# Kernel tuning notes

Measured on AMD Instinct MI355X. Metric: run time of the kernel, lower is better.

The kernel has to match this reference:

```python
import jax, jax.numpy as jnp
import numpy as np

B, S, SE, D, V, L, H = 32, 256, 1024, 512, 8000, 4, 8
EPS = 1e-3   # keras BatchNormalization default epsilon
NEG = -1e9


def _heads(x, W, b):
    Bx, Sx, Dx = x.shape
    return (jnp.einsum('bsd,de->bse', x, W) + b).reshape(Bx, Sx, H, Dx // H).transpose(0, 2, 1, 3)


def mha(q_in, kv_in, Wq, bq, Wk, bk, Wv, bv, Wo, bo, causal):
    dk = q_in.shape[-1] // H
    q = _heads(q_in, Wq, bq)   # [B,H,Sq,dk]
    k = _heads(kv_in, Wk, bk)  # [B,H,Sk,dk]
    v = _heads(kv_in, Wv, bv)
    scores = jnp.einsum('bhqd,bhkd->bhqk', q, k) / jnp.sqrt(jnp.asarray(dk, q.dtype))
    if causal:
        # original loop uses values = x[:, :j, :] -> token j attends to STRICTLY previous tokens;
        # token 0 has zero keys, so its attention output is exactly zero (before Wo bias).
        Sq, Sk = scores.shape[-2], scores.shape[-1]
        mask = jnp.arange(Sk)[None, :] < jnp.arange(Sq)[:, None]
        attn = jax.nn.softmax(jnp.where(mask, scores, NEG), axis=-1)
        attn = jnp.where(mask, attn, 0.0)
    else:
        attn = jax.nn.softmax(scores, axis=-1)
    out = jnp.einsum('bhqk,bhkd->bhqd', attn, v)
    out = out.transpose(0, 2, 1, 3).reshape(q_in.shape[0], q_in.shape[1], -1)
    return out @ Wo + bo


def bn(x, gamma, beta, mean, var):
    # keras BatchNorm, inference mode, axis=-1
    return gamma * (x - mean) * jax.lax.rsqrt(var + EPS) + beta


def setup_inputs():
    key = jax.random.key(0)
    ks = iter(jax.random.split(key, 80))

    def rn(*shape):
        return jax.random.normal(next(ks), shape, jnp.float32) * 0.02

    inp = {
        'sequence': jax.random.randint(next(ks), (B, S), 0, V, jnp.int32),
        'encoder_output': jax.random.normal(next(ks), (B, SE, D), jnp.float32),
        'pos_encodings': jax.random.normal(next(ks), (S, D), jnp.float32),
        'emb': rn(V, D),
        'Wout': rn(D, V), 'bout': jnp.zeros((V,), jnp.float32),
        'W1': rn(L, D, 512), 'b1': jnp.zeros((L, 512), jnp.float32),
        'W2': rn(L, 512, D), 'b2': jnp.zeros((L, D), jnp.float32),
    }
    for p in ('bot', 'mid'):
        for nm in ('Wq', 'Wk', 'Wv', 'Wo'):
            inp[f'{nm}_{p}'] = rn(L, D, D)
        for nm in ('bq', 'bk', 'bv', 'bo'):
            inp[f'{nm}_{p}'] = jnp.zeros((L, D), jnp.float32)
    for p in ('bot', 'mid', 'ffn'):
        inp[f'gamma_{p}'] = jnp.ones((L, D), jnp.float32)
        inp[f'beta_{p}'] = jnp.zeros((L, D), jnp.float32)
        inp[f'mean_{p}'] = jnp.zeros((L, D), jnp.float32)
        inp[f'var_{p}'] = jnp.ones((L, D), jnp.float32)
    return inp


def reference(sequence, encoder_output, pos_encodings, emb, Wout, bout, W1, b1, W2, b2,
              Wq_bot, Wk_bot, Wv_bot, Wo_bot, bq_bot, bk_bot, bv_bot, bo_bot,
              Wq_mid, Wk_mid, Wv_mid, Wo_mid, bq_mid, bk_mid, bv_mid, bo_mid,
              gamma_bot, beta_bot, mean_bot, var_bot,
              gamma_mid, beta_mid, mean_mid, var_mid,
              gamma_ffn, beta_ffn, mean_ffn, var_ffn):
    x = emb[sequence] + pos_encodings[None, :, :]  # [B,S,D]
    for i in range(L):
        a = mha(x, x, Wq_bot[i], bq_bot[i], Wk_bot[i], bk_bot[i], Wv_bot[i], bv_bot[i], Wo_bot[i], bo_bot[i], True)
        x = bn(x + a, gamma_bot[i], beta_bot[i], mean_bot[i], var_bot[i])
        a = mha(x, encoder_output, Wq_mid[i], bq_mid[i], Wk_mid[i], bk_mid[i], Wv_mid[i], bv_mid[i], Wo_mid[i], bo_mid[i], False)
        x = bn(x + a, gamma_mid[i], beta_mid[i], mean_mid[i], var_mid[i])
        f = jax.nn.relu(x @ W1[i] + b1[i]) @ W2[i] + b2[i]
        x = bn(x + f, gamma_ffn[i], beta_ffn[i], mean_ffn[i], var_ffn[i])
    return x @ Wout + bout  # logits [B,S,V]
```

## Files before the change

### kernel.cpp

```cpp
#include <hip/hip_runtime.h>
#include <hip/hip_fp16.h>

typedef _Float16 half8 __attribute__((ext_vector_type(8)));
typedef _Float16 half4 __attribute__((ext_vector_type(4)));
typedef float floatx4 __attribute__((ext_vector_type(4)));

#define NB 32
#define NS 256
#define NSE 1024
#define ND 512
#define NV 8000
#define NVP 8064
#define NL 4
#define NH 8
#define NDK 64
#define BN_EPS 1e-3f

typedef const __attribute__((address_space(1))) void* gas_ptr;
typedef __attribute__((address_space(3))) void* las_ptr;
__device__ __forceinline__ void gload16(const void* g, void* l) {
    __builtin_amdgcn_global_load_lds((gas_ptr)g, (las_ptr)l, 16, 0, 0);
}

__global__ __launch_bounds__(256) void k_cast(const float* __restrict__ in, _Float16* __restrict__ out) {
    size_t i = ((size_t)blockIdx.x * 256 + threadIdx.x) * 8;
    float4 a = *(const float4*)(in + i);
    float4 b = *(const float4*)(in + i + 4);
    half8 o;
    o[0] = (_Float16)a.x; o[1] = (_Float16)a.y; o[2] = (_Float16)a.z; o[3] = (_Float16)a.w;
    o[4] = (_Float16)b.x; o[5] = (_Float16)b.y; o[6] = (_Float16)b.z; o[7] = (_Float16)b.w;
    *(half8*)(out + i) = o;
}

__global__ __launch_bounds__(256) void k_embed(const int* __restrict__ seq,
                                               const float* __restrict__ emb,
                                               const float* __restrict__ pos,
                                               _Float16* __restrict__ x) {
    size_t i = ((size_t)blockIdx.x * 256 + threadIdx.x) * 8;
    int tok = (int)(i / ND);
    int d = (int)(i % ND);
    int s = tok % NS;
    int t = seq[tok];
    const float* ep = emb + (size_t)t * ND + d;
    const float* pp = pos + (size_t)s * ND + d;
    half8 o;
    for (int j = 0; j < 8; j++) o[j] = (_Float16)(ep[j] + pp[j]);
    *(half8*)(x + i) = o;
}

__global__ void k_transpose_w(const float* __restrict__ in, _Float16* __restrict__ out, int R, int C,
                              long long ostride) {
    __shared__ float tile[32][33];
    int b = blockIdx.z;
    int c0 = blockIdx.x * 32, r0 = blockIdx.y * 32;
    const float* pin = in + (size_t)b * R * C;
    _Float16* pout = out + (size_t)b * ostride;
    int tx = threadIdx.x, ty = threadIdx.y;
    for (int j = 0; j < 32; j += 8)
        tile[ty + j][tx] = pin[(size_t)(r0 + ty + j) * C + c0 + tx];
    __syncthreads();
    for (int j = 0; j < 32; j += 8)
        pout[(size_t)(c0 + ty + j) * R + r0 + tx] = (_Float16)tile[tx][ty + j];
}

template<int BM>
__global__ __launch_bounds__(256) void k_gemm(
    const _Float16* __restrict__ A, const _Float16* __restrict__ Bt,
    const float* __restrict__ bias0, const float* __restrict__ bias1, const float* __restrict__ bias2,
    void* __restrict__ C0, void* __restrict__ C1, void* __restrict__ C2,
    int M, int N, int K, int relu, int mode, int Sb,
    const _Float16* __restrict__ xres,
    const float* __restrict__ bng, const float* __restrict__ bnb,
    const float* __restrict__ bnm, const float* __restrict__ bnv) {
    constexpr int BN = 128;
    constexpr int BK = 64;
    constexpr int MI = BM / 32;
    constexpr int BUFH = (BM + BN) * BK;
    constexpr int LA = (BM + BN) / 32;
    __shared__ __align__(16) _Float16 smem[2 * BUFH];

    int tid = threadIdx.x;
    int wid = tid >> 6, lane = tid & 63, quad = lane >> 4, r = lane & 15;

    int nwg = gridDim.x * gridDim.y;
    int orig = blockIdx.y * gridDim.x + blockIdx.x;
    int q8 = nwg >> 3, r8 = nwg & 7;
    int xcd = orig & 7, loc = orig >> 3;
    int swz = (xcd < r8 ? xcd * (q8 + 1) : r8 * (q8 + 1) + (xcd - r8) * q8) + loc;
    int m0 = (swz / gridDim.x) * BM;
    int n0 = (swz % gridDim.x) * BN;

    int wm = (wid >> 1) * (BM / 2);
    int wn = (wid & 1) * 64;

    floatx4 zf = {0.f, 0.f, 0.f, 0.f};
    floatx4 acc[MI][4];
    for (int i = 0; i < MI; i++) for (int j = 0; j < 4; j++) acc[i][j] = zf;

    int srow = wid * 8 + (lane >> 3);
    int scol = (((lane & 7) ^ ((lane >> 3) & 7)) << 3);

    auto stage = [&](int k0, int buf) {
        _Float16* As = smem + buf * BUFH;
        _Float16* Bs = As + BM * BK;
        const _Float16* abase = A + (size_t)(m0 + srow) * K + k0 + scol;
        _Float16* asl = As + (wid * 8) * BK;
#pragma unroll
        for (int i = 0; i < BM / 32; i++)
            gload16(abase + (size_t)(i * 32) * K, asl + (i * 32) * BK);
        const _Float16* bbase = Bt + (size_t)(n0 + srow) * K + k0 + scol;
        _Float16* bsl = Bs + (wid * 8) * BK;
#pragma unroll
        for (int i = 0; i < 4; i++)
            gload16(bbase + (size_t)(i * 32) * K, bsl + (i * 32) * BK);
    };

    int NT = K / BK;
    int cur = 0;
    stage(0, 0);
    for (int t = 0; t < NT; t++) {
        if (t + 1 < NT) {
            stage((t + 1) * BK, cur ^ 1);
            asm volatile("s_waitcnt vmcnt(%0)" :: "n"(LA) : "memory");
        } else {
            asm volatile("s_waitcnt vmcnt(0)" ::: "memory");
        }
        __builtin_amdgcn_s_barrier();
        const _Float16* As = smem + cur * BUFH;
        const _Float16* Bs = As + BM * BK;
#pragma unroll
        for (int ks = 0; ks < BK; ks += 32) {
            half8 af[MI], bg[4];
#pragma unroll
            for (int i = 0; i < MI; i++)
                af[i] = *(const half8*)&As[(wm + i * 16 + r) * BK + ((((ks >> 3) + quad) ^ (r & 7)) << 3)];
#pragma unroll
            for (int j = 0; j < 4; j++)
                bg[j] = *(const half8*)&Bs[(wn + j * 16 + r) * BK + ((((ks >> 3) + quad) ^ (r & 7)) << 3)];
#pragma unroll
            for (int i = 0; i < MI; i++)
#pragma unroll
                for (int j = 0; j < 4; j++)
                    acc[i][j] = __builtin_amdgcn_mfma_f32_16x16x32_f16(af[i], bg[j], acc[i][j], 0, 0, 0);
        }
        if (t + 1 < NT) {
            __builtin_amdgcn_s_barrier();
            cur ^= 1;
        }
    }

    int seg = 0, nloc = n0, om = mode;
    const float* bias = bias0;
    char* C = (char*)C0;
    if (mode == 4) {
        seg = n0 >> 9; nloc = n0 & 511;
        om = (seg == 2) ? 1 : 0;
        C = (char*)(seg == 0 ? C0 : (seg == 1 ? C1 : C2));
        bias = (seg == 0) ? bias0 : ((seg == 1) ? bias1 : bias2);
    } else if (mode == 5) {
        seg = n0 >> 9; nloc = n0 & 511;
        om = seg ? 1 : 0;
        C = (char*)(seg ? C1 : C0);
        bias = seg ? bias1 : bias0;
    }

    if (om == 1) {
        for (int i = 0; i < MI; i++) {
            int grow = m0 + wm + i * 16 + quad * 4;
            int b = grow / Sb, s = grow - b * Sb;
            _Float16* outp = (_Float16*)C + (size_t)b * 512 * Sb + s;
#pragma unroll
            for (int j = 0; j < 4; j++) {
                int cb = nloc + wn + j * 16 + r;
                float bv = bias[cb];
                half4 h;
#pragma unroll
                for (int g = 0; g < 4; g++) h[g] = (_Float16)(acc[i][j][g] + bv);
                *(half4*)(outp + (size_t)cb * Sb) = h;
            }
        }
    } else {
        float* Ep = (float*)(void*)(smem + (cur ^ 1) * BUFH) + wid * (16 * 68);
        int rr = lane >> 4;
        int c = (lane & 15) * 4;
        for (int i = 0; i < MI; i++) {
#pragma unroll
            for (int j = 0; j < 4; j++) {
                int cb = nloc + wn + j * 16 + r;
                float bv = (om == 2) ? (cb < N ? bias[cb] : 0.0f) : bias[cb];
#pragma unroll
                for (int g = 0; g < 4; g++) {
                    float v = acc[i][j][g] + bv;
                    if (relu) v = fmaxf(v, 0.0f);
                    Ep[(quad * 4 + g) * 68 + j * 16 + r] = v;
                }
            }
            int grow0 = m0 + wm + i * 16;
            int cb = nloc + wn + c;
            if (om == 0) {
#pragma unroll
                for (int p = 0; p < 4; p++) {
                    float4 v = *(float4*)&Ep[(p * 4 + rr) * 68 + c];
                    half4 h;
                    h[0] = (_Float16)v.x; h[1] = (_Float16)v.y; h[2] = (_Float16)v.z; h[3] = (_Float16)v.w;
                    *(half4*)&((_Float16*)C)[(size_t)(grow0 + p * 4 + rr) * 512 + cb] = h;
                }
            } else if (om == 3) {
                float4 g4 = *(const float4*)(bng + cb);
                float4 b4 = *(const float4*)(bnb + cb);
                float4 m4 = *(const float4*)(bnm + cb);
                float4 v4 = *(const float4*)(bnv + cb);
                float s0 = g4.x * rsqrtf(v4.x + BN_EPS);
                float s1 = g4.y * rsqrtf(v4.y + BN_EPS);
                float s2 = g4.z * rsqrtf(v4.z + BN_EPS);
                float s3 = g4.w * rsqrtf(v4.w + BN_EPS);
#pragma unroll
                for (int p = 0; p < 4; p++) {
                    int grow = grow0 + p * 4 + rr;
                    float4 v = *(float4*)&Ep[(p * 4 + rr) * 68 + c];
                    half4 xv = *(const half4*)(xres + (size_t)grow * 512 + cb);
                    half4 h;
                    h[0] = (_Float16)((v.x + (float)xv[0] - m4.x) * s0 + b4.x);
                    h[1] = (_Float16)((v.y + (float)xv[1] - m4.y) * s1 + b4.y);
                    h[2] = (_Float16)((v.z + (float)xv[2] - m4.z) * s2 + b4.z);
                    h[3] = (_Float16)((v.w + (float)xv[3] - m4.w) * s3 + b4.w);
                    *(half4*)&((_Float16*)C)[(size_t)grow * 512 + cb] = h;
                }
            } else {
                if (cb < N) {
#pragma unroll
                    for (int p = 0; p < 4; p++) {
                        float4 v = *(float4*)&Ep[(p * 4 + rr) * 68 + c];
                        *(float4*)&((float*)C)[(size_t)(grow0 + p * 4 + rr) * N + cb] = v;
                    }
                }
            }
        }
    }
}

__global__ __launch_bounds__(256) void k_attn(const _Float16* __restrict__ Q, const _Float16* __restrict__ Kb,
                                              const _Float16* __restrict__ Vt, _Float16* __restrict__ O,
                                              int Sk, int causal) {
    __shared__ _Float16 Plds[4][16][72];
    int qt = blockIdx.x, h = blockIdx.y, b = blockIdx.z;
    int tid = threadIdx.x;
    int w = tid >> 6, lane = tid & 63, quad = lane >> 4, r = lane & 15;
    int qbase = qt * 64 + w * 16;

    floatx4 zf = {0.f, 0.f, 0.f, 0.f};
    half8 aq[2];
    const _Float16* qptr = Q + (size_t)(b * NS + qbase + r) * ND + h * NDK;
    aq[0] = *(const half8*)(qptr + quad * 8);
    aq[1] = *(const half8*)(qptr + 32 + quad * 8);

    floatx4 Of[4];
    for (int j = 0; j < 4; j++) Of[j] = zf;
    float mrow[4], lrow[4];
    for (int g = 0; g < 4; g++) { mrow[g] = -1e30f; lrow[g] = 0.0f; }

    int ntiles = causal ? (qt + 1) : (Sk >> 6);

    for (int kt = 0; kt < ntiles; kt++) {
        floatx4 sc[4];
        for (int j = 0; j < 4; j++) sc[j] = zf;
        for (int t = 0; t < 2; t++) {
            for (int j = 0; j < 4; j++) {
                const _Float16* kptr = Kb + (size_t)(b * Sk + kt * 64 + j * 16 + r) * ND + h * NDK + t * 32 + quad * 8;
                half8 bk = *(const half8*)kptr;
                sc[j] = __builtin_amdgcn_mfma_f32_16x16x32_f16(aq[t], bk, sc[j], 0, 0, 0);
            }
        }
        float s[4][4], tmax[4];
        for (int g = 0; g < 4; g++) tmax[g] = -1e30f;
        for (int j = 0; j < 4; j++) {
            int key = kt * 64 + j * 16 + r;
            for (int g = 0; g < 4; g++) {
                float v = sc[j][g] * 0.125f;
                int qi = qbase + quad * 4 + g;
                if (causal && key >= qi) v = -1e30f;
                s[j][g] = v;
                tmax[g] = fmaxf(tmax[g], v);
            }
        }
        for (int off = 1; off < 16; off <<= 1)
            for (int g = 0; g < 4; g++)
                tmax[g] = fmaxf(tmax[g], __shfl_xor(tmax[g], off, 64));
        float alpha[4], psum[4];
        for (int g = 0; g < 4; g++) {
            float mnew = fmaxf(mrow[g], tmax[g]);
            alpha[g] = (mnew <= -1e29f) ? 1.0f : __expf(mrow[g] - mnew);
            mrow[g] = mnew;
            psum[g] = 0.0f;
        }
        for (int j = 0; j < 4; j++) {
            for (int g = 0; g < 4; g++) {
                float p = (s[j][g] <= -1e29f) ? 0.0f : __expf(s[j][g] - mrow[g]);
                psum[g] += p;
                Plds[w][quad * 4 + g][j * 16 + r] = (_Float16)p;
            }
        }
        for (int off = 1; off < 16; off <<= 1)
            for (int g = 0; g < 4; g++)
                psum[g] += __shfl_xor(psum[g], off, 64);
        for (int g = 0; g < 4; g++) lrow[g] = lrow[g] * alpha[g] + psum[g];
        for (int j = 0; j < 4; j++)
            for (int g = 0; g < 4; g++)
                Of[j][g] *= alpha[g];
        __syncthreads();
        for (int t = 0; t < 2; t++) {
            half8 ap = *(const half8*)&Plds[w][r][t * 32 + quad * 8];
            for (int j = 0; j < 4; j++) {
                const _Float16* vptr = Vt + (size_t)((b * NH + h) * NDK + j * 16 + r) * Sk + kt * 64 + t * 32 + quad * 8;
                half8 bv = *(const half8*)vptr;
                Of[j] = __builtin_amdgcn_mfma_f32_16x16x32_f16(ap, bv, Of[j], 0, 0, 0);
            }
        }
        __syncthreads();
    }
    for (int j = 0; j < 4; j++) {
        for (int g = 0; g < 4; g++) {
            int row = qbase + quad * 4 + g;
            float inv = (lrow[g] > 0.f) ? 1.0f / lrow[g] : 0.0f;
            O[(size_t)(b * NS + row) * ND + h * NDK + j * 16 + r] = (_Float16)(Of[j][g] * inv);
        }
    }
}

extern "C" void kernel_launch(void* const* d_in, const int* in_sizes, int n_in,
                              void* d_out, int out_size, void* d_ws, size_t ws_size,
                              hipStream_t stream) {
    const int*   seq  = (const int*)d_in[0];
    const float* enc  = (const float*)d_in[1];
    const float* pos  = (const float*)d_in[2];
    const float* emb  = (const float*)d_in[3];
    const float* Wout = (const float*)d_in[4];
    const float* bout = (const float*)d_in[5];
    const float* W1   = (const float*)d_in[6];
    const float* b1   = (const float*)d_in[7];
    const float* W2   = (const float*)d_in[8];
    const float* b2   = (const float*)d_in[9];
    const float* Wq_bot = (const float*)d_in[10];
    const float* Wk_bot = (const float*)d_in[11];
    const float* Wv_bot = (const float*)d_in[12];
    const float* Wo_bot = (const float*)d_in[13];
    const float* bq_bot = (const float*)d_in[14];
    const float* bk_bot = (const float*)d_in[15];
    const float* bv_bot = (const float*)d_in[16];
    const float* bo_bot = (const float*)d_in[17];
    const float* Wq_mid = (const float*)d_in[18];
    const float* Wk_mid = (const float*)d_in[19];
    const float* Wv_mid = (const float*)d_in[20];
    const float* Wo_mid = (const float*)d_in[21];
    const float* bq_mid = (const float*)d_in[22];
    const float* bk_mid = (const float*)d_in[23];
    const float* bv_mid = (const float*)d_in[24];
    const float* bo_mid = (const float*)d_in[25];
    const float* gam[3] = {(const float*)d_in[26], (const float*)d_in[30], (const float*)d_in[34]};
    const float* bet[3] = {(const float*)d_in[27], (const float*)d_in[31], (const float*)d_in[35]};
    const float* mea[3] = {(const float*)d_in[28], (const float*)d_in[32], (const float*)d_in[36]};
    const float* vr [3] = {(const float*)d_in[29], (const float*)d_in[33], (const float*)d_in[37]};

    char* wp = (char*)d_ws;
    auto alloc = [&](size_t elems) -> _Float16* {
        _Float16* p = (_Float16*)wp;
        wp += ((elems * 2 + 255) / 256) * 256;
        return p;
    };
    const size_t DD = (size_t)ND * ND;
    _Float16* WqkvTb = alloc(NL * 3 * DD);
    _Float16* WoTb   = alloc(NL * DD);
    _Float16* WqTm   = alloc(NL * DD);
    _Float16* WkvTm  = alloc(NL * 2 * DD);
    _Float16* WoTm   = alloc(NL * DD);
    _Float16* W1T    = alloc(NL * DD);
    _Float16* W2T    = alloc(NL * DD);
    _Float16* WoutT  = alloc((size_t)NVP * ND);
    const size_t XSZ = (size_t)NB * NS * ND;
    _Float16* x   = alloc(XSZ);
    _Float16* qb  = alloc(XSZ);
    _Float16* kb  = alloc(XSZ);
    _Float16* vts = alloc(XSZ);
    _Float16* ao  = alloc(XSZ);
    const size_t ESZ = (size_t)NB * NSE * ND;
    _Float16* ench  = alloc(ESZ);
    _Float16* kenc  = alloc(ESZ);
    _Float16* vtenc = alloc(ESZ);

    hipMemsetAsync(WoutT + (size_t)NV * ND, 0, (size_t)(NVP - NV) * ND * sizeof(_Float16), stream);

    dim3 tb(32, 8);
    const long long S1 = (long long)DD, S2 = (long long)(2 * DD), S3 = (long long)(3 * DD);
    k_transpose_w<<<dim3(16, 16, NL), tb, 0, stream>>>(Wq_bot, WqkvTb,          ND, ND, S3);
    k_transpose_w<<<dim3(16, 16, NL), tb, 0, stream>>>(Wk_bot, WqkvTb + DD,     ND, ND, S3);
    k_transpose_w<<<dim3(16, 16, NL), tb, 0, stream>>>(Wv_bot, WqkvTb + 2 * DD, ND, ND, S3);
    k_transpose_w<<<dim3(16, 16, NL), tb, 0, stream>>>(Wo_bot, WoTb,            ND, ND, S1);
    k_transpose_w<<<dim3(16, 16, NL), tb, 0, stream>>>(Wq_mid, WqTm,            ND, ND, S1);
    k_transpose_w<<<dim3(16, 16, NL), tb, 0, stream>>>(Wk_mid, WkvTm,           ND, ND, S2);
    k_transpose_w<<<dim3(16, 16, NL), tb, 0, stream>>>(Wv_mid, WkvTm + DD,      ND, ND, S2);
    k_transpose_w<<<dim3(16, 16, NL), tb, 0, stream>>>(Wo_mid, WoTm,            ND, ND, S1);
    k_transpose_w<<<dim3(16, 16, NL), tb, 0, stream>>>(W1,     W1T,             ND, ND, S1);
    k_transpose_w<<<dim3(16, 16, NL), tb, 0, stream>>>(W2,     W2T,             ND, ND, S1);
    k_transpose_w<<<dim3(NV / 32, 16, 1), tb, 0, stream>>>(Wout, WoutT, ND, NV, S1);
    k_cast<<<dim3((int)(ESZ / 8 / 256)), 256, 0, stream>>>(enc, ench);
    k_embed<<<dim3((int)(XSZ / 8 / 256)), 256, 0, stream>>>(seq, emb, pos, x);

    auto gemm64 = [&](const _Float16* A, const _Float16* Bt, const float* b0, void* Cp,
                      int relu, int mode, const _Float16* xr, const float* g, const float* be,
                      const float* me, const float* ve) {
        k_gemm<64><<<dim3(4, 128), 256, 0, stream>>>(A, Bt, b0, nullptr, nullptr,
            Cp, nullptr, nullptr, 8192, 512, 512, relu, mode, 0, xr, g, be, me, ve);
    };

    for (int l = 0; l < NL; l++) {
        size_t wofs = (size_t)l * DD;
        size_t bofs = (size_t)l * ND;
        k_gemm<128><<<dim3(12, 64), 256, 0, stream>>>(x, WqkvTb + (size_t)l * 3 * DD,
            bq_bot + bofs, bk_bot + bofs, bv_bot + bofs, qb, kb, vts,
            8192, 1536, 512, 0, 4, NS, nullptr, nullptr, nullptr, nullptr, nullptr);
        k_attn<<<dim3(NS / 64, NH, NB), 256, 0, stream>>>(qb, kb, vts, ao, NS, 1);
        gemm64(ao, WoTb + wofs, bo_bot + bofs, x, 0, 3, x,
               gam[0] + bofs, bet[0] + bofs, mea[0] + bofs, vr[0] + bofs);
        gemm64(x, WqTm + wofs, bq_mid + bofs, qb, 0, 0, nullptr, nullptr, nullptr, nullptr, nullptr);
        k_gemm<128><<<dim3(8, 256), 256, 0, stream>>>(ench, WkvTm + (size_t)l * 2 * DD,
            bk_mid + bofs, bv_mid + bofs, nullptr, kenc, vtenc, nullptr,
            32768, 1024, 512, 0, 5, NSE, nullptr, nullptr, nullptr, nullptr, nullptr);
        k_attn<<<dim3(NS / 64, NH, NB), 256, 0, stream>>>(qb, kenc, vtenc, ao, NSE, 0);
        gemm64(ao, WoTm + wofs, bo_mid + bofs, x, 0, 3, x,
               gam[1] + bofs, bet[1] + bofs, mea[1] + bofs, vr[1] + bofs);
        gemm64(x, W1T + wofs, b1 + bofs, qb, 1, 0, nullptr, nullptr, nullptr, nullptr, nullptr);
        gemm64(qb, W2T + wofs, b2 + bofs, x, 0, 3, x,
               gam[2] + bofs, bet[2] + bofs, mea[2] + bofs, vr[2] + bofs);
    }
    k_gemm<128><<<dim3(63, 64), 256, 0, stream>>>(x, WoutT, bout, nullptr, nullptr,
        d_out, nullptr, nullptr, 8192, NV, 512, 0, 2, 0, nullptr, nullptr, nullptr, nullptr, nullptr);
}
```

Measured before the change: 1.765 ms.

## Widen attention KV tiles, stage transposed GEMM stores via LDS, batch weight transposes

Attention now processes 128 keys per tile instead of 64, which halves the number of softmax rescale and barrier iterations. It also fully unrolls the inner loops and raises wave priority around the MFMA sections. The BM=128 GEMM path that writes head-transposed outputs now stages results in swizzled LDS, so each global store becomes a coalesced 16-byte write instead of a strided 8-byte one. The ten per-weight transpose launches are merged into one kernel launch. Costs are higher register pressure from 8 score accumulators and extra causal work on partially masked 128-wide tiles.

```diff
diff --git a/kernel.cpp b/kernel.cpp
--- a/kernel.cpp
+++ b/kernel.cpp
@@ -14,6 +14,7 @@
 #define NL 4
 #define NH 8
 #define NDK 64
+#define KVB 128
 #define BN_EPS 1e-3f
 
 typedef const __attribute__((address_space(1))) void* gas_ptr;
@@ -61,6 +62,26 @@
     __syncthreads();
     for (int j = 0; j < 32; j += 8)
         pout[(size_t)(c0 + ty + j) * R + r0 + tx] = (_Float16)tile[tx][ty + j];
+}
+
+struct TWArgs {
+    const float* src[10];
+    _Float16* dst[10];
+    long long ostride[10];
+};
+__global__ void k_transpose_all(TWArgs a) {
+    __shared__ float tile[32][33];
+    int z = blockIdx.z;
+    int g = z >> 2, l = z & 3;
+    const float* pin = a.src[g] + (size_t)l * ND * ND;
+    _Float16* pout = a.dst[g] + (size_t)l * a.ostride[g];
+    int c0 = blockIdx.x * 32, r0 = blockIdx.y * 32;
+    int tx = threadIdx.x, ty = threadIdx.y;
+    for (int j = 0; j < 32; j += 8)
+        tile[ty + j][tx] = pin[(size_t)(r0 + ty + j) * ND + c0 + tx];
+    __syncthreads();
+    for (int j = 0; j < 32; j += 8)
+        pout[(size_t)(c0 + ty + j) * ND + r0 + tx] = (_Float16)tile[tx][ty + j];
 }
 
 template<int BM>
@@ -165,18 +186,51 @@
     }
 
     if (om == 1) {
-        for (int i = 0; i < MI; i++) {
-            int grow = m0 + wm + i * 16 + quad * 4;
-            int b = grow / Sb, s = grow - b * Sb;
-            _Float16* outp = (_Float16*)C + (size_t)b * 512 * Sb + s;
-#pragma unroll
-            for (int j = 0; j < 4; j++) {
-                int cb = nloc + wn + j * 16 + r;
-                float bv = bias[cb];
-                half4 h;
-#pragma unroll
-                for (int g = 0; g < 4; g++) h[g] = (_Float16)(acc[i][j][g] + bv);
-                *(half4*)(outp + (size_t)cb * Sb) = h;
+        if constexpr (BM == 128) {
+            _Float16* Lt = smem + (cur ^ 1) * BUFH;
+            for (int i = 0; i < MI; i++) {
+                int sl = wm + i * 16 + quad * 4;
+                int cs = sl >> 2;
+#pragma unroll
+                for (int j = 0; j < 4; j++) {
+                    int cl = wn + j * 16 + r;
+                    float bv = bias[nloc + cl];
+                    half4 h;
+#pragma unroll
+                    for (int g = 0; g < 4; g++) h[g] = (_Float16)(acc[i][j][g] + bv);
+                    *(half4*)&Lt[cl * BM + ((cs ^ (cl & 7)) << 2)] = h;
+                }
+            }
+            __syncthreads();
+            int b = m0 / Sb, s0 = m0 - b * Sb;
+            _Float16* outb = (_Float16*)C + (size_t)b * 512 * Sb + s0;
+            int tcol = tid >> 4;
+            int ts8 = (tid & 15) * 8;
+            int cs0 = ts8 >> 2;
+#pragma unroll
+            for (int p = 0; p < 8; p++) {
+                int cl = p * 16 + tcol;
+                half4 lo = *(const half4*)&Lt[cl * BM + ((cs0 ^ (cl & 7)) << 2)];
+                half4 hi = *(const half4*)&Lt[cl * BM + (((cs0 + 1) ^ (cl & 7)) << 2)];
+                half8 o;
+                o[0] = lo[0]; o[1] = lo[1]; o[2] = lo[2]; o[3] = lo[3];
+                o[4] = hi[0]; o[5] = hi[1]; o[6] = hi[2]; o[7] = hi[3];
+                *(half8*)&outb[(size_t)(nloc + cl) * Sb + ts8] = o;
+            }
+        } else {
+            for (int i = 0; i < MI; i++) {
+                int grow = m0 + wm + i * 16 + quad * 4;
+                int b = grow / Sb, s = grow - b * Sb;
+                _Float16* outp = (_Float16*)C + (size_t)b * 512 * Sb + s;
+#pragma unroll
+                for (int j = 0; j < 4; j++) {
+                    int cb = nloc + wn + j * 16 + r;
+                    float bv = bias[cb];
+                    half4 h;
+#pragma unroll
+                    for (int g = 0; g < 4; g++) h[g] = (_Float16)(acc[i][j][g] + bv);
+                    *(half4*)(outp + (size_t)cb * Sb) = h;
+                }
             }
         }
     } else {
@@ -242,7 +296,7 @@
 __global__ __launch_bounds__(256) void k_attn(const _Float16* __restrict__ Q, const _Float16* __restrict__ Kb,
                                               const _Float16* __restrict__ Vt, _Float16* __restrict__ O,
                                               int Sk, int causal) {
-    __shared__ _Float16 Plds[4][16][72];
+    __shared__ _Float16 Plds[4][16][KVB + 8];
     int qt = blockIdx.x, h = blockIdx.y, b = blockIdx.z;
     int tid = threadIdx.x;
     int w = tid >> 6, lane = tid & 63, quad = lane >> 4, r = lane & 15;
@@ -259,22 +313,30 @@
     float mrow[4], lrow[4];
     for (int g = 0; g < 4; g++) { mrow[g] = -1e30f; lrow[g] = 0.0f; }
 
-    int ntiles = causal ? (qt + 1) : (Sk >> 6);
+    int ntiles = causal ? ((qt * 64 + 63) / KVB + 1) : (Sk / KVB);
 
     for (int kt = 0; kt < ntiles; kt++) {
-        floatx4 sc[4];
-        for (int j = 0; j < 4; j++) sc[j] = zf;
+        floatx4 sc[8];
+#pragma unroll
+        for (int j = 0; j < 8; j++) sc[j] = zf;
+        __builtin_amdgcn_s_setprio(1);
+#pragma unroll
         for (int t = 0; t < 2; t++) {
-            for (int j = 0; j < 4; j++) {
-                const _Float16* kptr = Kb + (size_t)(b * Sk + kt * 64 + j * 16 + r) * ND + h * NDK + t * 32 + quad * 8;
+#pragma unroll
+            for (int j = 0; j < 8; j++) {
+                const _Float16* kptr = Kb + (size_t)(b * Sk + kt * KVB + j * 16 + r) * ND + h * NDK + t * 32 + quad * 8;
                 half8 bk = *(const half8*)kptr;
                 sc[j] = __builtin_amdgcn_mfma_f32_16x16x32_f16(aq[t], bk, sc[j], 0, 0, 0);
             }
         }
-        float s[4][4], tmax[4];
+        __builtin_amdgcn_s_setprio(0);
+        float s[8][4], tmax[4];
+#pragma unroll
         for (int g = 0; g < 4; g++) tmax[g] = -1e30f;
-        for (int j = 0; j < 4; j++) {
-            int key = kt * 64 + j * 16 + r;
+#pragma unroll
+        for (int j = 0; j < 8; j++) {
+            int key = kt * KVB + j * 16 + r;
+#pragma unroll
             for (int g = 0; g < 4; g++) {
                 float v = sc[j][g] * 0.125f;
                 int qi = qbase + quad * 4 + g;
@@ -283,39 +345,53 @@
                 tmax[g] = fmaxf(tmax[g], v);
             }
         }
+#pragma unroll
         for (int off = 1; off < 16; off <<= 1)
+#pragma unroll
             for (int g = 0; g < 4; g++)
                 tmax[g] = fmaxf(tmax[g], __shfl_xor(tmax[g], off, 64));
         float alpha[4], psum[4];
+#pragma unroll
         for (int g = 0; g < 4; g++) {
             float mnew = fmaxf(mrow[g], tmax[g]);
             alpha[g] = (mnew <= -1e29f) ? 1.0f : __expf(mrow[g] - mnew);
             mrow[g] = mnew;
             psum[g] = 0.0f;
         }
-        for (int j = 0; j < 4; j++) {
+#pragma unroll
+        for (int j = 0; j < 8; j++) {
+#pragma unroll
             for (int g = 0; g < 4; g++) {
                 float p = (s[j][g] <= -1e29f) ? 0.0f : __expf(s[j][g] - mrow[g]);
                 psum[g] += p;
                 Plds[w][quad * 4 + g][j * 16 + r] = (_Float16)p;
             }
         }
+#pragma unroll
         for (int off = 1; off < 16; off <<= 1)
+#pragma unroll
             for (int g = 0; g < 4; g++)
                 psum[g] += __shfl_xor(psum[g], off, 64);
+#pragma unroll
         for (int g = 0; g < 4; g++) lrow[g] = lrow[g] * alpha[g] + psum[g];
+#pragma unroll
         for (int j = 0; j < 4; j++)
+#pragma unroll
             for (int g = 0; g < 4; g++)
                 Of[j][g] *= alpha[g];
         __syncthreads();
-        for (int t = 0; t < 2; t++) {
+        __builtin_amdgcn_s_setprio(1);
+#pragma unroll
+        for (int t = 0; t < 4; t++) {
             half8 ap = *(const half8*)&Plds[w][r][t * 32 + quad * 8];
+#pragma unroll
             for (int j = 0; j < 4; j++) {
-                const _Float16* vptr = Vt + (size_t)((b * NH + h) * NDK + j * 16 + r) * Sk + kt * 64 + t * 32 + quad * 8;
+                const _Float16* vptr = Vt + (size_t)((b * NH + h) * NDK + j * 16 + r) * Sk + kt * KVB + t * 32 + quad * 8;
                 half8 bv = *(const half8*)vptr;
                 Of[j] = __builtin_amdgcn_mfma_f32_16x16x32_f16(ap, bv, Of[j], 0, 0, 0);
             }
         }
+        __builtin_amdgcn_s_setprio(0);
         __syncthreads();
     }
     for (int j = 0; j < 4; j++) {
@@ -391,16 +467,18 @@
 
     dim3 tb(32, 8);
     const long long S1 = (long long)DD, S2 = (long long)(2 * DD), S3 = (long long)(3 * DD);
-    k_transpose_w<<<dim3(16, 16, NL), tb, 0, stream>>>(Wq_bot, WqkvTb,          ND, ND, S3);
-    k_transpose_w<<<dim3(16, 16, NL), tb, 0, stream>>>(Wk_bot, WqkvTb + DD,     ND, ND, S3);
-    k_transpose_w<<<dim3(16, 16, NL), tb, 0, stream>>>(Wv_bot, WqkvTb + 2 * DD, ND, ND, S3);
-    k_transpose_w<<<dim3(16, 16, NL), tb, 0, stream>>>(Wo_bot, WoTb,            ND, ND, S1);
-    k_transpose_w<<<dim3(16, 16, NL), tb, 0, stream>>>(Wq_mid, WqTm,            ND, ND, S1);
-    k_transpose_w<<<dim3(16, 16, NL), tb, 0, stream>>>(Wk_mid, WkvTm,           ND, ND, S2);
-    k_transpose_w<<<dim3(16, 16, NL), tb, 0, stream>>>(Wv_mid, WkvTm + DD,      ND, ND, S2);
-    k_transpose_w<<<dim3(16, 16, NL), tb, 0, stream>>>(Wo_mid, WoTm,            ND, ND, S1);
-    k_transpose_w<<<dim3(16, 16, NL), tb, 0, stream>>>(W1,     W1T,             ND, ND, S1);
-    k_transpose_w<<<dim3(16, 16, NL), tb, 0, stream>>>(W2,     W2T,             ND, ND, S1);
+    TWArgs ta;
+    ta.src[0] = Wq_bot; ta.dst[0] = WqkvTb;          ta.ostride[0] = S3;
+    ta.src[1] = Wk_bot; ta.dst[1] = WqkvTb + DD;     ta.ostride[1] = S3;
+    ta.src[2] = Wv_bot; ta.dst[2] = WqkvTb + 2 * DD; ta.ostride[2] = S3;
+    ta.src[3] = Wo_bot; ta.dst[3] = WoTb;            ta.ostride[3] = S1;
+    ta.src[4] = Wq_mid; ta.dst[4] = WqTm;            ta.ostride[4] = S1;
+    ta.src[5] = Wk_mid; ta.dst[5] = WkvTm;           ta.ostride[5] = S2;
+    ta.src[6] = Wv_mid; ta.dst[6] = WkvTm + DD;      ta.ostride[6] = S2;
+    ta.src[7] = Wo_mid; ta.dst[7] = WoTm;            ta.ostride[7] = S1;
+    ta.src[8] = W1;     ta.dst[8] = W1T;             ta.ostride[8] = S1;
+    ta.src[9] = W2;     ta.dst[9] = W2T;             ta.ostride[9] = S1;
+    k_transpose_all<<<dim3(16, 16, 40), tb, 0, stream>>>(ta);
     k_transpose_w<<<dim3(NV / 32, 16, 1), tb, 0, stream>>>(Wout, WoutT, ND, NV, S1);
     k_cast<<<dim3((int)(ESZ / 8 / 256)), 256, 0, stream>>>(enc, ench);
     k_embed<<<dim3((int)(XSZ / 8 / 256)), 256, 0, stream>>>(seq, emb, pos, x);
```

New measurement: 2.045 ms. 15.9% more time.
